# Kernel optimization log

Hardware: AMD Instinct MI355X
Metric: run time of the kernel (lower is better)

Reference implementation:

```python
import jax, jax.numpy as jnp
import numpy as np

THRESHOLD_HU = 50.0
BASE_THR = THRESHOLD_HU / 255.0  # normalized threshold
LEVELS = 3
INV_SQRT2 = 0.7071067811865476


def setup_inputs() -> dict:
    key = jax.random.key(0)
    pred = jax.random.normal(key, (64, 1, 1024, 1024), dtype=jnp.float32)
    return {"pred": pred}


def _haar_dwt2(x):
    """One level of 2D Haar DWT on x [B,H,W] (pywt 'haar', even sizes).
    Returns (LL, LH, HL, HH). Sign conventions don't affect the loss
    (it only depends on |coeff|)."""
    lo = (x[:, 0::2, :] + x[:, 1::2, :]) * INV_SQRT2  # rows lowpass  [B,H/2,W]
    hi = (x[:, 1::2, :] - x[:, 0::2, :]) * INV_SQRT2  # rows highpass [B,H/2,W]
    ll = (lo[:, :, 0::2] + lo[:, :, 1::2]) * INV_SQRT2
    lh = (lo[:, :, 1::2] - lo[:, :, 0::2]) * INV_SQRT2
    hl = (hi[:, :, 0::2] + hi[:, :, 1::2]) * INV_SQRT2
    hh = (hi[:, :, 1::2] - hi[:, :, 0::2]) * INV_SQRT2
    return ll, lh, hl, hh


def _band_loss(c, thr):
    # L1(c, soft_threshold(c, thr)) = mean(min(|c|, thr))
    return jnp.mean(jnp.minimum(jnp.abs(c), thr))


def reference(pred):
    # pred: [B, C, H, W]; only channel 0 is used (as in the torch module).
    x = pred[:, 0]  # [B, H, W]
    total = jnp.zeros((), dtype=pred.dtype)
    # decomposition step j=1 is the finest detail (pywt level_idx = LEVELS),
    # step j=LEVELS is the coarsest (pywt level_idx = 1).
    for j in range(1, LEVELS + 1):
        x, lh, hl, hh = _haar_dwt2(x)
        level_idx = LEVELS - j + 1
        thr = BASE_THR / (2.0 ** (level_idx - 1))
        level_weight = 1.0 / level_idx
        band = (_band_loss(lh, thr) + _band_loss(hl, thr) + _band_loss(hh, thr)) / 3.0
        total = total + level_weight * band
    # per-sample means are identical-shape, so mean over batch is already
    # folded into the band means; valid_samples == B for finite inputs.
    return total
```

## Files before the change

### kernel.cpp

```cpp
#include <hip/hip_runtime.h>


#define NBLK 4096

static __device__ __forceinline__ float band3(float lh, float hl, float hh, float thr) {
    return fminf(fabsf(lh), thr) + fminf(fabsf(hl), thr) + fminf(fabsf(hh), thr);
}

__global__ __launch_bounds__(256) void wsp_partial(const float* __restrict__ pred,
                                                   float* __restrict__ partial) {
    const int tid = blockIdx.x * 256 + threadIdx.x;
    const int tx = tid & 127;
    const int ty = (tid >> 7) & 127;
    const int b  = tid >> 14;

    const float* base = pred + ((size_t)b << 20) + ((size_t)ty << 13) + ((size_t)tx << 3);

    const float T1 = (50.0f / 255.0f) * 0.25f;
    const float T2 = (50.0f / 255.0f) * 0.5f;
    const float T3 = (50.0f / 255.0f);

    float ll1[4][4];
    float s1 = 0.0f, s2 = 0.0f, s3 = 0.0f;

    #pragma unroll
    for (int r = 0; r < 4; ++r) {
        const float* r0 = base + ((size_t)(2 * r) << 10);
        const float* r1 = r0 + 1024;
        float4 a0 = *reinterpret_cast<const float4*>(r0);
        float4 a1 = *reinterpret_cast<const float4*>(r0 + 4);
        float4 b0 = *reinterpret_cast<const float4*>(r1);
        float4 b1 = *reinterpret_cast<const float4*>(r1 + 4);
        float lo[8], hi[8];
        lo[0] = a0.x + b0.x; hi[0] = b0.x - a0.x;
        lo[1] = a0.y + b0.y; hi[1] = b0.y - a0.y;
        lo[2] = a0.z + b0.z; hi[2] = b0.z - a0.z;
        lo[3] = a0.w + b0.w; hi[3] = b0.w - a0.w;
        lo[4] = a1.x + b1.x; hi[4] = b1.x - a1.x;
        lo[5] = a1.y + b1.y; hi[5] = b1.y - a1.y;
        lo[6] = a1.z + b1.z; hi[6] = b1.z - a1.z;
        lo[7] = a1.w + b1.w; hi[7] = b1.w - a1.w;
        #pragma unroll
        for (int c = 0; c < 4; ++c) {
            float ll = (lo[2 * c] + lo[2 * c + 1]) * 0.5f;
            float lh = (lo[2 * c + 1] - lo[2 * c]) * 0.5f;
            float hl = (hi[2 * c] + hi[2 * c + 1]) * 0.5f;
            float hh = (hi[2 * c + 1] - hi[2 * c]) * 0.5f;
            s1 += band3(lh, hl, hh, T1);
            ll1[r][c] = ll;
        }
    }

    float ll2[2][2];
    #pragma unroll
    for (int r = 0; r < 2; ++r) {
        float lo[4], hi[4];
        #pragma unroll
        for (int c = 0; c < 4; ++c) {
            lo[c] = ll1[2 * r][c] + ll1[2 * r + 1][c];
            hi[c] = ll1[2 * r + 1][c] - ll1[2 * r][c];
        }
        #pragma unroll
        for (int c = 0; c < 2; ++c) {
            float ll = (lo[2 * c] + lo[2 * c + 1]) * 0.5f;
            float lh = (lo[2 * c + 1] - lo[2 * c]) * 0.5f;
            float hl = (hi[2 * c] + hi[2 * c + 1]) * 0.5f;
            float hh = (hi[2 * c + 1] - hi[2 * c]) * 0.5f;
            s2 += band3(lh, hl, hh, T2);
            ll2[r][c] = ll;
        }
    }

    {
        float lo0 = ll2[0][0] + ll2[1][0];
        float lo1 = ll2[0][1] + ll2[1][1];
        float hi0 = ll2[1][0] - ll2[0][0];
        float hi1 = ll2[1][1] - ll2[0][1];
        float lh = (lo1 - lo0) * 0.5f;
        float hl = (hi0 + hi1) * 0.5f;
        float hh = (hi1 - hi0) * 0.5f;
        s3 = band3(lh, hl, hh, T3);
    }

    const float A1 = 1.0f / 150994944.0f;
    const float A2 = 1.0f / 25165824.0f;
    const float A3 = 1.0f / 3145728.0f;
    float c = s1 * A1 + s2 * A2 + s3 * A3;

    __shared__ float red[256];
    red[threadIdx.x] = c;
    __syncthreads();
    #pragma unroll
    for (int off = 128; off > 0; off >>= 1) {
        if (threadIdx.x < off) red[threadIdx.x] += red[threadIdx.x + off];
        __syncthreads();
    }
    if (threadIdx.x == 0) partial[blockIdx.x] = red[0];
}

__global__ __launch_bounds__(256) void wsp_reduce(const float* __restrict__ partial,
                                                  float* __restrict__ out) {
    __shared__ float red[256];
    float s = 0.0f;
    for (int i = threadIdx.x; i < NBLK; i += 256) s += partial[i];
    red[threadIdx.x] = s;
    __syncthreads();
    #pragma unroll
    for (int off = 128; off > 0; off >>= 1) {
        if (threadIdx.x < off) red[threadIdx.x] += red[threadIdx.x + off];
        __syncthreads();
    }
    if (threadIdx.x == 0) out[0] = red[0];
}

extern "C" void kernel_launch(void* const* d_in, const int* in_sizes, int n_in,
                              void* d_out, int out_size, void* d_ws, size_t ws_size,
                              hipStream_t stream) {
    const float* pred = (const float*)d_in[0];
    float* partial = (float*)d_ws;
    float* out = (float*)d_out;

    wsp_partial<<<NBLK, 256, 0, stream>>>(pred, partial);
    wsp_reduce<<<1, 256, 0, stream>>>(partial, out);
}
```

Measured before the change: 48.87 us.

## Process two tiles per thread, use nontemporal loads, fold Haar scaling into thresholds

Each thread now handles two adjacent 8x8 tiles, and the grid is halved so fewer blocks and partials are produced. Input loads use nontemporal builtins, which hint the hardware not to keep the streamed data in cache. The per-level 0.5 Haar scaling is removed and folded into rescaled thresholds and weights, which drops several multiplies per coefficient. Per-thread work and register use go up, and the access pattern changes: each thread's 16 contiguous floats per row are read as four float4 loads.

```diff
diff --git a/kernel.cpp b/kernel.cpp
--- a/kernel.cpp
+++ b/kernel.cpp
@@ -1,53 +1,46 @@
 #include <hip/hip_runtime.h>
 
 
-#define NBLK 4096
+#define NBLK 2048
+
+typedef float floatx4 __attribute__((ext_vector_type(4)));
+
+#define BASE_THR (50.0f / 255.0f)
+#define T1P (BASE_THR * 0.5f)
+#define T2P (BASE_THR * 2.0f)
+#define T3P (BASE_THR * 8.0f)
+#define A1P (1.0f / 301989888.0f)
+#define A2P (1.0f / 100663296.0f)
+#define A3P (1.0f / 25165824.0f)
 
 static __device__ __forceinline__ float band3(float lh, float hl, float hh, float thr) {
     return fminf(fabsf(lh), thr) + fminf(fabsf(hl), thr) + fminf(fabsf(hh), thr);
 }
 
-__global__ __launch_bounds__(256) void wsp_partial(const float* __restrict__ pred,
-                                                   float* __restrict__ partial) {
-    const int tid = blockIdx.x * 256 + threadIdx.x;
-    const int tx = tid & 127;
-    const int ty = (tid >> 7) & 127;
-    const int b  = tid >> 14;
-
-    const float* base = pred + ((size_t)b << 20) + ((size_t)ty << 13) + ((size_t)tx << 3);
-
-    const float T1 = (50.0f / 255.0f) * 0.25f;
-    const float T2 = (50.0f / 255.0f) * 0.5f;
-    const float T3 = (50.0f / 255.0f);
-
+static __device__ __forceinline__ float tile_loss(const float* __restrict__ base) {
     float ll1[4][4];
     float s1 = 0.0f, s2 = 0.0f, s3 = 0.0f;
 
     #pragma unroll
     for (int r = 0; r < 4; ++r) {
         const float* r0 = base + ((size_t)(2 * r) << 10);
-        const float* r1 = r0 + 1024;
-        float4 a0 = *reinterpret_cast<const float4*>(r0);
-        float4 a1 = *reinterpret_cast<const float4*>(r0 + 4);
-        float4 b0 = *reinterpret_cast<const float4*>(r1);
-        float4 b1 = *reinterpret_cast<const float4*>(r1 + 4);
+        floatx4 a0 = __builtin_nontemporal_load(reinterpret_cast<const floatx4*>(r0));
+        floatx4 a1 = __builtin_nontemporal_load(reinterpret_cast<const floatx4*>(r0 + 4));
+        floatx4 b0 = __builtin_nontemporal_load(reinterpret_cast<const floatx4*>(r0 + 1024));
+        floatx4 b1 = __builtin_nontemporal_load(reinterpret_cast<const floatx4*>(r0 + 1028));
         float lo[8], hi[8];
-        lo[0] = a0.x + b0.x; hi[0] = b0.x - a0.x;
-        lo[1] = a0.y + b0.y; hi[1] = b0.y - a0.y;
-        lo[2] = a0.z + b0.z; hi[2] = b0.z - a0.z;
-        lo[3] = a0.w + b0.w; hi[3] = b0.w - a0.w;
-        lo[4] = a1.x + b1.x; hi[4] = b1.x - a1.x;
-        lo[5] = a1.y + b1.y; hi[5] = b1.y - a1.y;
-        lo[6] = a1.z + b1.z; hi[6] = b1.z - a1.z;
-        lo[7] = a1.w + b1.w; hi[7] = b1.w - a1.w;
+        #pragma unroll
+        for (int k = 0; k < 4; ++k) {
+            lo[k]     = a0[k] + b0[k]; hi[k]     = b0[k] - a0[k];
+            lo[k + 4] = a1[k] + b1[k]; hi[k + 4] = b1[k] - a1[k];
+        }
         #pragma unroll
         for (int c = 0; c < 4; ++c) {
-            float ll = (lo[2 * c] + lo[2 * c + 1]) * 0.5f;
-            float lh = (lo[2 * c + 1] - lo[2 * c]) * 0.5f;
-            float hl = (hi[2 * c] + hi[2 * c + 1]) * 0.5f;
-            float hh = (hi[2 * c + 1] - hi[2 * c]) * 0.5f;
-            s1 += band3(lh, hl, hh, T1);
-            ll1[r][c] = ll;
+            ll1[r][c] = lo[2 * c] + lo[2 * c + 1];
+            float lh = lo[2 * c + 1] - lo[2 * c];
+            float hl = hi[2 * c] + hi[2 * c + 1];
+            float hh = hi[2 * c + 1] - hi[2 * c];
+            s1 += band3(lh, hl, hh, T1P);
         }
     }
 
@@ -62,12 +55,11 @@
         }
         #pragma unroll
         for (int c = 0; c < 2; ++c) {
-            float ll = (lo[2 * c] + lo[2 * c + 1]) * 0.5f;
-            float lh = (lo[2 * c + 1] - lo[2 * c]) * 0.5f;
-            float hl = (hi[2 * c] + hi[2 * c + 1]) * 0.5f;
-            float hh = (hi[2 * c + 1] - hi[2 * c]) * 0.5f;
-            s2 += band3(lh, hl, hh, T2);
-            ll2[r][c] = ll;
+            ll2[r][c] = lo[2 * c] + lo[2 * c + 1];
+            float lh = lo[2 * c + 1] - lo[2 * c];
+            float hl = hi[2 * c] + hi[2 * c + 1];
+            float hh = hi[2 * c + 1] - hi[2 * c];
+            s2 += band3(lh, hl, hh, T2P);
         }
     }
 
@@ -76,16 +68,25 @@
         float lo1 = ll2[0][1] + ll2[1][1];
         float hi0 = ll2[1][0] - ll2[0][0];
         float hi1 = ll2[1][1] - ll2[0][1];
-        float lh = (lo1 - lo0) * 0.5f;
-        float hl = (hi0 + hi1) * 0.5f;
-        float hh = (hi1 - hi0) * 0.5f;
-        s3 = band3(lh, hl, hh, T3);
+        float lh = lo1 - lo0;
+        float hl = hi0 + hi1;
+        float hh = hi1 - hi0;
+        s3 = band3(lh, hl, hh, T3P);
     }
 
-    const float A1 = 1.0f / 150994944.0f;
-    const float A2 = 1.0f / 25165824.0f;
-    const float A3 = 1.0f / 3145728.0f;
-    float c = s1 * A1 + s2 * A2 + s3 * A3;
+    return s1 * A1P + s2 * A2P + s3 * A3P;
+}
+
+__global__ __launch_bounds__(256) void wsp_partial(const float* __restrict__ pred,
+                                                   float* __restrict__ partial) {
+    const int tid = blockIdx.x * 256 + threadIdx.x;
+    const int tx = tid & 63;
+    const int ty = (tid >> 6) & 127;
+    const int b  = tid >> 13;
+
+    const float* base = pred + ((size_t)b << 20) + ((size_t)ty << 13) + ((size_t)tx << 4);
+
+    float c = tile_loss(base) + tile_loss(base + 8);
 
     __shared__ float red[256];
     red[threadIdx.x] = c;
```

Measured after the change: 100.9 us. 107% more time.
